# Performance work log

Measured on AMD Instinct MI355X. Metric: run time of the kernel, lower is better.

Reference implementation:

```python
import jax, jax.numpy as jnp
import numpy as np

SEMA_DIM = 1024
L1, L2, B = 256, 320, 64


def setup_inputs() -> dict:
    key = jax.random.key(0)
    k1, k2, kw1, kb1, kw2, kb2 = jax.random.split(key, 6)
    D = SEMA_DIM
    s = 1.0 / np.sqrt(D)
    return {
        "r1": jax.random.normal(k1, (L1, B, D), dtype=jnp.float32),
        "r2": jax.random.normal(k2, (L2, B, D), dtype=jnp.float32),
        "W1": jax.random.uniform(kw1, (D, D), jnp.float32, -s, s),
        "b1": jax.random.uniform(kb1, (D,), jnp.float32, -s, s),
        "W2": jax.random.uniform(kw2, (D, D), jnp.float32, -s, s),
        "b2": jax.random.uniform(kb2, (D,), jnp.float32, -s, s),
    }


def _mlp(x, W1, b1, W2, b2):
    # torch Linear: x @ W.T + b
    h = jax.nn.relu(x @ W1.T + b1)
    return h @ W2.T + b2


def reference(r1, r2, W1, b1, W2, b2):
    # (L, B, D) -> mlp -> (B, L, D)
    r1 = jnp.transpose(_mlp(r1, W1, b1, W2, b2), (1, 0, 2))  # [B, L1, D]
    r2 = jnp.transpose(_mlp(r2, W1, b1, W2, b2), (1, 0, 2))  # [B, L2, D]

    o = jnp.einsum("bid,bjd->bij", r1, r2)  # [B, L1, L2]
    o1 = jax.nn.softmax(o, axis=2)           # attend r1 -> r2
    o2 = jax.nn.softmax(o, axis=1)           # attend r2 -> r1

    r1_c = jnp.einsum("bij,bjd->bid", o1, r2)  # [B, L1, D]
    r2_c = jnp.einsum("bij,bid->bjd", o2, r1)  # [B, L2, D]

    r1_pool = jnp.concatenate([r1, r1_c], axis=-1).sum(axis=1) / r1.shape[1]  # [B, 2D]
    r2_pool = jnp.concatenate([r2, r2_c], axis=-1).sum(axis=1) / r2.shape[1]  # [B, 2D]
    return (r1_pool, r2_pool)
```

## Files before the change

### kernel.cpp

```cpp
#include <hip/hip_runtime.h>
#include <stdint.h>

#define L1C 256
#define L2C 320
#define BC  64
#define DC  1024

typedef __bf16 bf16_t;
typedef __bf16 bf16x8 __attribute__((ext_vector_type(8)));
typedef __bf16 bf16x4 __attribute__((ext_vector_type(4)));
typedef float  f32x4  __attribute__((ext_vector_type(4)));

__device__ __forceinline__ void gload16(const void* g, void* l) {
  __builtin_amdgcn_global_load_lds(
      (__attribute__((address_space(1))) void*)g,
      (__attribute__((address_space(3))) void*)l, 16, 0, 0);
}

__global__ __launch_bounds__(256)
void conv_kernel(const float* __restrict__ src, bf16_t* __restrict__ dst, int n4) {
  int i = blockIdx.x * 256 + threadIdx.x;
  const int stride = gridDim.x * 256;
  for (; i < n4; i += stride) {
    float4 v = ((const float4*)src)[i];
    bf16x4 o = { (__bf16)v.x, (__bf16)v.y, (__bf16)v.z, (__bf16)v.w };
    ((bf16x4*)dst)[i] = o;
  }
}

__global__ __launch_bounds__(256)
void mlp_gemm(const bf16_t* __restrict__ A, const bf16_t* __restrict__ W,
              const float* __restrict__ bias, bf16_t* __restrict__ C,
              int Mtiles, int relu) {
  const int nwg = Mtiles * 8;
  const int wg  = ((int)blockIdx.x & 7) * (nwg >> 3) + ((int)blockIdx.x >> 3);
  const int mt = wg >> 3, nt = wg & 7;

  const int f = threadIdx.x;
  const int lane = f & 63, w = f >> 6;
  const int sRow = f >> 2, sCol8 = (f & 3) * 8;

  const bf16_t* Ab = A + (size_t)mt * 128 * 1024 + (size_t)sRow * 1024 + sCol8;
  const bf16_t* Bb = W + (size_t)nt * 128 * 1024 + (size_t)sRow * 1024 + sCol8;

  __shared__ __align__(16) bf16_t sA[128 * 32];
  __shared__ __align__(16) bf16_t sB[128 * 32];
  bf16_t* sAp = sA + sRow * 32 + sCol8;
  bf16_t* sBp = sB + sRow * 32 + sCol8;

  const int wr = (w >> 1) * 64, wc = (w & 1) * 64;
  const int rsel = lane & 15, koff = (lane >> 4) * 8;
  const bf16_t* rA = sA + (wr + rsel) * 32 + koff;
  const bf16_t* rB = sB + (wc + rsel) * 32 + koff;

  f32x4 acc[4][4] = {};
  for (int kt = 0; kt < 1024; kt += 32) {
    __syncthreads();
    gload16(Ab + kt,             sAp);
    gload16(Ab + kt + 64 * 1024, sAp + 64 * 32);
    gload16(Bb + kt,             sBp);
    gload16(Bb + kt + 64 * 1024, sBp + 64 * 32);
    asm volatile("s_waitcnt vmcnt(0)" ::: "memory");
    __syncthreads();
    bf16x8 af[4], bfv[4];
#pragma unroll
    for (int m = 0; m < 4; ++m) af[m] = *(const bf16x8*)(rA + m * 16 * 32);
#pragma unroll
    for (int n = 0; n < 4; ++n) bfv[n] = *(const bf16x8*)(rB + n * 16 * 32);
#pragma unroll
    for (int m = 0; m < 4; ++m)
#pragma unroll
      for (int n = 0; n < 4; ++n)
        acc[m][n] = __builtin_amdgcn_mfma_f32_16x16x32_bf16(af[m], bfv[n], acc[m][n], 0, 0, 0);
  }

  const int row0 = mt * 128 + wr + (lane >> 4) * 4;
  const int col0 = nt * 128 + wc + rsel;
#pragma unroll
  for (int n = 0; n < 4; ++n) {
    const int c = col0 + n * 16;
    const float bv = bias[c];
#pragma unroll
    for (int m = 0; m < 4; ++m) {
      const int r = row0 + m * 16;
#pragma unroll
      for (int q = 0; q < 4; ++q) {
        float v = acc[m][n][q] + bv;
        if (relu) v = fmaxf(v, 0.f);
        C[(size_t)(r + q) * 1024 + c] = (bf16_t)v;
      }
    }
  }
}

__global__ __launch_bounds__(256)
void logits_gemm(const bf16_t* __restrict__ Y, float* __restrict__ O) {
  const int wg = ((int)blockIdx.x & 7) * 48 + ((int)blockIdx.x >> 3);
  const int b = wg / 6, t = wg % 6;
  const int mt = t / 3, nt = t % 3;

  const int f = threadIdx.x;
  const int lane = f & 63, w = f >> 6;
  const int sRow = f >> 2, sCol8 = (f & 3) * 8;

  const bf16_t* Y1 = Y;
  const bf16_t* Y2 = Y + (size_t)L1C * BC * DC;

  const int i0 = mt * 128 + sRow;
  const int i1 = i0 + 64;
  int j0 = nt * 128 + sRow;      if (j0 > L2C - 1) j0 = L2C - 1;
  int j1 = nt * 128 + sRow + 64; if (j1 > L2C - 1) j1 = L2C - 1;
  const bf16_t* A0 = Y1 + ((size_t)i0 * BC + b) * DC + sCol8;
  const bf16_t* A1 = Y1 + ((size_t)i1 * BC + b) * DC + sCol8;
  const bf16_t* B0 = Y2 + ((size_t)j0 * BC + b) * DC + sCol8;
  const bf16_t* B1 = Y2 + ((size_t)j1 * BC + b) * DC + sCol8;

  __shared__ __align__(16) bf16_t sA[128 * 32];
  __shared__ __align__(16) bf16_t sB[128 * 32];
  bf16_t* sAp = sA + sRow * 32 + sCol8;
  bf16_t* sBp = sB + sRow * 32 + sCol8;

  const int wr = (w >> 1) * 64, wc = (w & 1) * 64;
  const int rsel = lane & 15, koff = (lane >> 4) * 8;
  const bf16_t* rA = sA + (wr + rsel) * 32 + koff;
  const bf16_t* rB = sB + (wc + rsel) * 32 + koff;

  f32x4 acc[4][4] = {};
  for (int kt = 0; kt < 1024; kt += 32) {
    __syncthreads();
    gload16(A0 + kt, sAp);
    gload16(A1 + kt, sAp + 64 * 32);
    gload16(B0 + kt, sBp);
    gload16(B1 + kt, sBp + 64 * 32);
    asm volatile("s_waitcnt vmcnt(0)" ::: "memory");
    __syncthreads();
    bf16x8 af[4], bfv[4];
#pragma unroll
    for (int m = 0; m < 4; ++m) af[m] = *(const bf16x8*)(rA + m * 16 * 32);
#pragma unroll
    for (int n = 0; n < 4; ++n) bfv[n] = *(const bf16x8*)(rB + n * 16 * 32);
#pragma unroll
    for (int m = 0; m < 4; ++m)
#pragma unroll
      for (int n = 0; n < 4; ++n)
        acc[m][n] = __builtin_amdgcn_mfma_f32_16x16x32_bf16(af[m], bfv[n], acc[m][n], 0, 0, 0);
  }

  float* Ob = O + (size_t)b * L1C * L2C;
  const int row0 = mt * 128 + wr + (lane >> 4) * 4;
  const int col0 = nt * 128 + wc + rsel;
#pragma unroll
  for (int n = 0; n < 4; ++n) {
    const int c = col0 + n * 16;
    if (c < L2C) {
#pragma unroll
      for (int m = 0; m < 4; ++m) {
        const int r = row0 + m * 16;
#pragma unroll
        for (int q = 0; q < 4; ++q)
          Ob[(size_t)(r + q) * L2C + c] = acc[m][n][q];
      }
    }
  }
}

__global__ __launch_bounds__(256)
void row_stats(const float* __restrict__ O, float* __restrict__ rowM,
               float* __restrict__ rowInv) {
  const int gw = blockIdx.x * 4 + (threadIdx.x >> 6);
  const int lane = threadIdx.x & 63;
  const float* row = O + (size_t)gw * L2C;
  float v[5];
  float m = -1e30f;
#pragma unroll
  for (int t = 0; t < 5; ++t) { v[t] = row[t * 64 + lane]; m = fmaxf(m, v[t]); }
#pragma unroll
  for (int off = 32; off; off >>= 1) m = fmaxf(m, __shfl_xor(m, off));
  float s = 0.f;
#pragma unroll
  for (int t = 0; t < 5; ++t) s += __expf(v[t] - m);
#pragma unroll
  for (int off = 32; off; off >>= 1) s += __shfl_xor(s, off);
  if (lane == 0) { rowM[gw] = m; rowInv[gw] = 1.f / s; }
}

__global__ __launch_bounds__(256)
void col_stats_c1(const float* __restrict__ O, const float* __restrict__ rowM,
                  const float* __restrict__ rowInv, float* __restrict__ colM,
                  float* __restrict__ colInv, float* __restrict__ c1) {
  const int b = blockIdx.x / 5, jb = blockIdx.x % 5;
  const int jl = threadIdx.x & 63, ig = threadIdx.x >> 6;
  const int j = jb * 64 + jl;
  const float* Ob = O + (size_t)b * L1C * L2C + j;
  const float* rM = rowM + b * L1C;
  const float* rI = rowInv + b * L1C;
  float m = -1e30f, s = 0.f, cp = 0.f;
  for (int i = ig; i < L1C; i += 4) {
    float v = Ob[(size_t)i * L2C];
    float mn = fmaxf(m, v);
    s = s * __expf(m - mn) + __expf(v - mn);
    m = mn;
    cp += __expf(v - rM[i]) * rI[i];
  }
  __shared__ float sm[4][64], ss[4][64], sc[4][64];
  sm[ig][jl] = m; ss[ig][jl] = s; sc[ig][jl] = cp;
  __syncthreads();
  if (ig == 0) {
    for (int g = 1; g < 4; ++g) {
      float mg = sm[g][jl], sg = ss[g][jl];
      float mn = fmaxf(m, mg);
      s = s * __expf(m - mn) + sg * __expf(mg - mn);
      m = mn;
      cp += sc[g][jl];
    }
    colM[b * L2C + j] = m;
    colInv[b * L2C + j] = 1.f / s;
    c1[b * L2C + j] = cp;
  }
}

__global__ __launch_bounds__(256)
void c2_kernel(const float* __restrict__ O, const float* __restrict__ colM,
               const float* __restrict__ colInv, float* __restrict__ c2) {
  const int gw = blockIdx.x * 4 + (threadIdx.x >> 6);
  const int lane = threadIdx.x & 63;
  const int b = gw >> 8;
  const float* row = O + (size_t)gw * L2C;
  const float* cM = colM + b * L2C;
  const float* cI = colInv + b * L2C;
  float s = 0.f;
#pragma unroll
  for (int t = 0; t < 5; ++t) {
    const int j = t * 64 + lane;
    s += __expf(row[j] - cM[j]) * cI[j];
  }
#pragma unroll
  for (int off = 32; off; off >>= 1) s += __shfl_xor(s, off);
  if (lane == 0) c2[gw] = s;
}

__global__ __launch_bounds__(256)
void pool_y1(const bf16_t* __restrict__ Y1, const float* __restrict__ c2,
             float* __restrict__ out) {
  const int b = blockIdx.x >> 2;
  const int d = (blockIdx.x & 3) * 256 + threadIdx.x;
  float s1 = 0.f, s2 = 0.f;
  const float* c2b = c2 + b * L1C;
  for (int i = 0; i < L1C; ++i) {
    float v = (float)Y1[((size_t)i * BC + b) * DC + d];
    s1 += v;
    s2 += c2b[i] * v;
  }
  out[(size_t)b * 2048 + d] = s1 * (1.f / L1C);
  out[(size_t)BC * 2048 + (size_t)b * 2048 + 1024 + d] = s2 * (1.f / L2C);
}

__global__ __launch_bounds__(256)
void pool_y2(const bf16_t* __restrict__ Y2, const float* __restrict__ c1,
             float* __restrict__ out) {
  const int b = blockIdx.x >> 2;
  const int d = (blockIdx.x & 3) * 256 + threadIdx.x;
  float s1 = 0.f, s2 = 0.f;
  const float* c1b = c1 + b * L2C;
  for (int j = 0; j < L2C; ++j) {
    float v = (float)Y2[((size_t)j * BC + b) * DC + d];
    s1 += v;
    s2 += c1b[j] * v;
  }
  out[(size_t)BC * 2048 + (size_t)b * 2048 + d] = s1 * (1.f / L2C);
  out[(size_t)b * 2048 + 1024 + d] = s2 * (1.f / L1C);
}

extern "C" void kernel_launch(void* const* d_in, const int* in_sizes, int n_in,
                              void* d_out, int out_size, void* d_ws, size_t ws_size,
                              hipStream_t stream) {
  const float* r1 = (const float*)d_in[0];
  const float* r2 = (const float*)d_in[1];
  const float* W1 = (const float*)d_in[2];
  const float* b1 = (const float*)d_in[3];
  const float* W2 = (const float*)d_in[4];
  const float* b2 = (const float*)d_in[5];
  float* out = (float*)d_out;
  char* ws = (char*)d_ws;

  const size_t M1 = (size_t)L1C * BC;
  const size_t M2 = (size_t)L2C * BC;
  const size_t Mt = M1 + M2;

  size_t off = 0;
  bf16_t* XB  = (bf16_t*)(ws + off); off += Mt * DC * 2;
  bf16_t* HB  = (bf16_t*)(ws + off); off += Mt * DC * 2;
  bf16_t* WB1 = (bf16_t*)(ws + off); off += (size_t)DC * DC * 2;
  bf16_t* WB2 = (bf16_t*)(ws + off); off += (size_t)DC * DC * 2;
  float* rowM   = (float*)(ws + off); off += 65536;
  float* rowInv = (float*)(ws + off); off += 65536;
  float* colM   = (float*)(ws + off); off += 81920;
  float* colInv = (float*)(ws + off); off += 81920;
  float* c1v    = (float*)(ws + off); off += 81920;
  float* c2v    = (float*)(ws + off); off += 65536;

  bf16_t* YB = XB;
  float*  O  = (float*)HB;

  conv_kernel<<<2048, 256, 0, stream>>>(r1, XB,            (int)(M1 * DC / 4));
  conv_kernel<<<2048, 256, 0, stream>>>(r2, XB + M1 * DC,  (int)(M2 * DC / 4));
  conv_kernel<<<512,  256, 0, stream>>>(W1, WB1, (int)((size_t)DC * DC / 4));
  conv_kernel<<<512,  256, 0, stream>>>(W2, WB2, (int)((size_t)DC * DC / 4));

  mlp_gemm<<<288 * 8, 256, 0, stream>>>(XB, WB1, b1, HB, 288, 1);
  mlp_gemm<<<288 * 8, 256, 0, stream>>>(HB, WB2, b2, YB, 288, 0);

  logits_gemm<<<384, 256, 0, stream>>>(YB, O);

  row_stats<<<4096, 256, 0, stream>>>(O, rowM, rowInv);
  col_stats_c1<<<320, 256, 0, stream>>>(O, rowM, rowInv, colM, colInv, c1v);
  c2_kernel<<<4096, 256, 0, stream>>>(O, colM, colInv, c2v);

  pool_y1<<<256, 256, 0, stream>>>(YB, c2v, out);
  pool_y2<<<256, 256, 0, stream>>>(YB + M1 * DC, c1v, out);
}
```

Measured before the change: 316.1 us.

## Rewrite MLP GEMM as 256x256-tile, 8-wave kernel with 4-stage LDS pipeline

Replaces the 128x128 single-buffered MLP GEMM with a 512-thread kernel computing 256x256 tiles. It uses a 4-slot LDS ring with async global->LDS loads issued three K-steps ahead, XOR-swizzled LDS layout to avoid bank conflicts, and split MFMA phases with s_setprio to overlap loads with compute. This targets the serialized load/wait/compute pattern and low operand reuse of the old kernel, at the cost of 128KB LDS per block and higher register pressure.

```diff
diff --git a/kernel.cpp b/kernel.cpp
--- a/kernel.cpp
+++ b/kernel.cpp
@@ -28,66 +28,110 @@
   }
 }
 
-__global__ __launch_bounds__(256)
-void mlp_gemm(const bf16_t* __restrict__ A, const bf16_t* __restrict__ W,
-              const float* __restrict__ bias, bf16_t* __restrict__ C,
-              int Mtiles, int relu) {
-  const int nwg = Mtiles * 8;
-  const int wg  = ((int)blockIdx.x & 7) * (nwg >> 3) + ((int)blockIdx.x >> 3);
-  const int mt = wg >> 3, nt = wg & 7;
-
-  const int f = threadIdx.x;
-  const int lane = f & 63, w = f >> 6;
-  const int sRow = f >> 2, sCol8 = (f & 3) * 8;
-
-  const bf16_t* Ab = A + (size_t)mt * 128 * 1024 + (size_t)sRow * 1024 + sCol8;
-  const bf16_t* Bb = W + (size_t)nt * 128 * 1024 + (size_t)sRow * 1024 + sCol8;
-
-  __shared__ __align__(16) bf16_t sA[128 * 32];
-  __shared__ __align__(16) bf16_t sB[128 * 32];
-  bf16_t* sAp = sA + sRow * 32 + sCol8;
-  bf16_t* sBp = sB + sRow * 32 + sCol8;
-
-  const int wr = (w >> 1) * 64, wc = (w & 1) * 64;
-  const int rsel = lane & 15, koff = (lane >> 4) * 8;
-  const bf16_t* rA = sA + (wr + rsel) * 32 + koff;
-  const bf16_t* rB = sB + (wc + rsel) * 32 + koff;
-
-  f32x4 acc[4][4] = {};
-  for (int kt = 0; kt < 1024; kt += 32) {
-    __syncthreads();
-    gload16(Ab + kt,             sAp);
-    gload16(Ab + kt + 64 * 1024, sAp + 64 * 32);
-    gload16(Bb + kt,             sBp);
-    gload16(Bb + kt + 64 * 1024, sBp + 64 * 32);
-    asm volatile("s_waitcnt vmcnt(0)" ::: "memory");
-    __syncthreads();
-    bf16x8 af[4], bfv[4];
-#pragma unroll
-    for (int m = 0; m < 4; ++m) af[m] = *(const bf16x8*)(rA + m * 16 * 32);
-#pragma unroll
-    for (int n = 0; n < 4; ++n) bfv[n] = *(const bf16x8*)(rB + n * 16 * 32);
+__global__ __launch_bounds__(512, 2)
+void mlp_gemm8(const bf16_t* __restrict__ A, const bf16_t* __restrict__ W,
+               const float* __restrict__ bias, bf16_t* __restrict__ C,
+               int Mtiles, int relu) {
+  const int nwg = Mtiles * 4;
+  const int cpx = nwg >> 3;
+  const int wg  = ((int)blockIdx.x & 7) * cpx + ((int)blockIdx.x >> 3);
+  const int mt = wg >> 2, nt = wg & 3;
+
+  __shared__ __align__(16) char lds[131072];
+
+  const int t    = threadIdx.x;
+  const int lane = t & 63, wid = t >> 6;
+  const int wm = wid >> 2, wn = wid & 3;
+  const int rsel = lane & 15, hi = lane >> 4;
+  const int t16 = t * 16;
+
+  const int P0 = t16, P1 = 8192 + t16;
+  const int Lg0 = P0 ^ ((P0 >> 3) & 0x30);
+  const int Lg1 = P1 ^ ((P1 >> 3) & 0x30);
+  const int rS0 = Lg0 >> 6, cS0 = (Lg0 & 63) >> 1;
+  const int rS1 = Lg1 >> 6, cS1 = (Lg1 & 63) >> 1;
+  const bf16_t* pA0 = A + (size_t)(mt * 256 + rS0) * 1024 + cS0;
+  const bf16_t* pA1 = A + (size_t)(mt * 256 + rS1) * 1024 + cS1;
+  const bf16_t* pB0 = W + (size_t)(nt * 256 + rS0) * 1024 + cS0;
+  const bf16_t* pB1 = W + (size_t)(nt * 256 + rS1) * 1024 + cS1;
+
+  const int kchunk = (hi ^ ((rsel >> 1) & 3)) << 4;
+  const int offA = ((wm * 128 + rsel) << 6) + kchunk;
+  const int offB = 16384 + ((wn * 64 + rsel) << 6) + kchunk;
+
+  f32x4 acc[8][4] = {};
+  bf16x8 bfr[4];
+
+#pragma unroll
+  for (int p = 0; p < 3; ++p) {
+    char* db = lds + p * 32768;
+    gload16(pA0 + p * 32, db + t16);
+    gload16(pA1 + p * 32, db + 8192 + t16);
+    gload16(pB0 + p * 32, db + 16384 + t16);
+    gload16(pB1 + p * 32, db + 24576 + t16);
+  }
+  asm volatile("s_waitcnt vmcnt(8)" ::: "memory");
+  __builtin_amdgcn_s_barrier();
+  __builtin_amdgcn_sched_barrier(0);
+
+#pragma unroll 1
+  for (int tt = 0; tt < 32; ++tt) {
+    const char* rb = lds + (tt & 3) * 32768;
+    char* sb = lds + ((tt + 3) & 3) * 32768;
+    const int ks = (tt + 3) * 32;
+    bf16x8 af[4];
+#pragma unroll
+    for (int m = 0; m < 4; ++m) af[m] = *(const bf16x8*)(rb + offA + m * 1024);
+#pragma unroll
+    for (int n = 0; n < 4; ++n) bfr[n] = *(const bf16x8*)(rb + offB + n * 1024);
+    if (tt < 29) {
+      gload16(pA0 + ks, sb + t16);
+      gload16(pA1 + ks, sb + 8192 + t16);
+    }
+    __builtin_amdgcn_s_setprio(1);
 #pragma unroll
     for (int m = 0; m < 4; ++m)
 #pragma unroll
       for (int n = 0; n < 4; ++n)
-        acc[m][n] = __builtin_amdgcn_mfma_f32_16x16x32_bf16(af[m], bfv[n], acc[m][n], 0, 0, 0);
-  }
-
-  const int row0 = mt * 128 + wr + (lane >> 4) * 4;
-  const int col0 = nt * 128 + wc + rsel;
-#pragma unroll
-  for (int n = 0; n < 4; ++n) {
-    const int c = col0 + n * 16;
-    const float bv = bias[c];
-#pragma unroll
-    for (int m = 0; m < 4; ++m) {
-      const int r = row0 + m * 16;
-#pragma unroll
-      for (int q = 0; q < 4; ++q) {
-        float v = acc[m][n][q] + bv;
+        acc[m][n] = __builtin_amdgcn_mfma_f32_16x16x32_bf16(af[m], bfr[n], acc[m][n], 0, 0, 0);
+    __builtin_amdgcn_s_setprio(0);
+    __builtin_amdgcn_s_barrier();
+    __builtin_amdgcn_sched_barrier(0);
+#pragma unroll
+    for (int m = 0; m < 4; ++m) af[m] = *(const bf16x8*)(rb + offA + (m + 4) * 1024);
+    if (tt < 29) {
+      gload16(pB0 + ks, sb + 16384 + t16);
+      gload16(pB1 + ks, sb + 24576 + t16);
+    }
+    __builtin_amdgcn_s_setprio(1);
+#pragma unroll
+    for (int m = 0; m < 4; ++m)
+#pragma unroll
+      for (int n = 0; n < 4; ++n)
+        acc[m + 4][n] = __builtin_amdgcn_mfma_f32_16x16x32_bf16(af[m], bfr[n], acc[m + 4][n], 0, 0, 0);
+    __builtin_amdgcn_s_setprio(0);
+    if (tt < 29)       asm volatile("s_waitcnt vmcnt(8)" ::: "memory");
+    else if (tt == 29) asm volatile("s_waitcnt vmcnt(4)" ::: "memory");
+    else if (tt == 30) asm volatile("s_waitcnt vmcnt(0)" ::: "memory");
+    __builtin_amdgcn_s_barrier();
+    __builtin_amdgcn_sched_barrier(0);
+  }
+
+  const int row0 = mt * 256 + wm * 128 + hi * 4;
+  const int col0 = nt * 256 + wn * 64 + rsel;
+  float bv[4];
+#pragma unroll
+  for (int n = 0; n < 4; ++n) bv[n] = bias[col0 + n * 16];
+#pragma unroll
+  for (int m = 0; m < 8; ++m) {
+#pragma unroll
+    for (int q = 0; q < 4; ++q) {
+      const size_t rr = (size_t)(row0 + m * 16 + q) * 1024;
+#pragma unroll
+      for (int n = 0; n < 4; ++n) {
+        float v = acc[m][n][q] + bv[n];
         if (relu) v = fmaxf(v, 0.f);
-        C[(size_t)(r + q) * 1024 + c] = (bf16_t)v;
+        C[rr + col0 + n * 16] = (bf16_t)v;
       }
     }
   }
@@ -307,8 +351,8 @@
   conv_kernel<<<512,  256, 0, stream>>>(W1, WB1, (int)((size_t)DC * DC / 4));
   conv_kernel<<<512,  256, 0, stream>>>(W2, WB2, (int)((size_t)DC * DC / 4));
 
-  mlp_gemm<<<288 * 8, 256, 0, stream>>>(XB, WB1, b1, HB, 288, 1);
-  mlp_gemm<<<288 * 8, 256, 0, stream>>>(HB, WB2, b2, YB, 288, 0);
+  mlp_gemm8<<<576, 512, 0, stream>>>(XB, WB1, b1, HB, 144, 1);
+  mlp_gemm8<<<576, 512, 0, stream>>>(HB, WB2, b2, YB, 144, 0);
 
   logits_gemm<<<384, 256, 0, stream>>>(YB, O);
 
```

Measured after the change: 331.2 us. 1.05x slower.
